# Kernel optimization log

Measured on AMD Instinct MI355X. Metric: run time of the kernel, lower is better.

## Reference

```python
import jax, jax.numpy as jnp
import numpy as np

N, K = 16384, 25
D_SELF, D_NEIGH, D_LINK, D_OUT = 256, 256, 64, 256


def _glorot(key, shape):
    fan = shape[0] if len(shape) == 1 else (shape[0] + shape[1])
    limit = np.sqrt(6.0 / fan).astype(np.float32)
    return jax.random.uniform(key, shape, jnp.float32, -limit, limit)


def setup_inputs() -> dict:
    key = jax.random.key(0)
    ks = jax.random.split(key, 10)
    return {
        "self_vecs": jax.random.normal(ks[0], (N, D_SELF), jnp.float32),
        "neigh_vecs": jax.random.normal(ks[1], (N, K, D_NEIGH), jnp.float32),
        "link_vecs": jax.random.normal(ks[2], (N, K, D_LINK), jnp.float32),
        # keep probs away from 0 to avoid huge 1/p values
        "select_probs": jax.random.uniform(ks[3], (N, K), jnp.float32) * 0.9 + 0.1,
        # Gate parameters (weight vectors)
        "g_self_w": _glorot(ks[4], (D_SELF,)),
        "g_neigh_w": _glorot(ks[5], (D_NEIGH,)),
        "g_link_w": _glorot(ks[6], (D_LINK,)),
        # Aggregator parameters
        "W_link": _glorot(ks[7], (D_LINK, D_NEIGH)),
        "W_self": _glorot(ks[8], (D_SELF, D_OUT)),
        "W_neigh": _glorot(ks[9], (D_NEIGH, D_OUT)),
    }


def reference(self_vecs, neigh_vecs, link_vecs, select_probs,
              g_self_w, g_neigh_w, g_link_w, W_link, W_self, W_neigh):
    # dropout = 0.0 -> identity
    # Gate: sigmoid(trans_self[:, None] + trans_neigh + trans_link)  -> [N, K]
    trans_self = self_vecs @ g_self_w                                  # [N]
    trans_neigh = jnp.einsum('nkd,d->nk', neigh_vecs, g_neigh_w)       # [N, K]
    trans_link = jnp.einsum('nkl,l->nk', link_vecs, g_link_w)          # [N, K]
    gate = jax.nn.sigmoid(trans_self[:, None] + trans_neigh + trans_link)

    # link-conditioned amplification of neighbor features
    trans_links = jax.nn.sigmoid(jnp.einsum('nkl,ld->nkd', link_vecs, W_link))  # [N, K, D_NEIGH]
    amplified = neigh_vecs * trans_links

    # select_probs provided -> gate/prob weighting and mean over neighbors
    w = gate / select_probs                                            # [N, K]
    expected = jnp.mean(amplified * w[..., None], axis=-2)             # [N, D_NEIGH]

    from_self = self_vecs @ W_self                                     # [N, D_OUT]
    from_neighs = expected @ W_neigh                                   # [N, D_OUT]
    out = jnp.concatenate([from_self, from_neighs], axis=-1)           # concat combination
    return jax.nn.relu(out)
```

## Files before the change

kernel.cpp:

```cpp
#include <hip/hip_runtime.h>

#define DEV __device__ __forceinline__

typedef __bf16 bf16;
typedef bf16 bf16x4 __attribute__((ext_vector_type(4)));
typedef bf16 bf16x8 __attribute__((ext_vector_type(8)));
typedef float f32x4 __attribute__((ext_vector_type(4)));

constexpr int N_NODES = 16384;
constexpr int KN = 25;
constexpr int DS = 256, DN = 256, DL = 64;

constexpr size_t WS_WLT  = 0;
constexpr size_t WS_WCAT = 32768;
constexpr size_t WS_EXP  = 32768 + 262144;

DEV float sigmoid_fast(float x) {
    return __builtin_amdgcn_rcpf(1.0f + __builtin_amdgcn_exp2f(-1.44269504088896341f * x));
}

__global__ void prep_kernel(const float* __restrict__ W_link,
                            const float* __restrict__ W_self,
                            const float* __restrict__ W_neigh,
                            bf16* __restrict__ wlT, bf16* __restrict__ wcat) {
    int tid = blockIdx.x * blockDim.x + threadIdx.x;
    int stride = gridDim.x * blockDim.x;
    for (int i = tid; i < DL * DN; i += stride) {
        int d = i >> 6, l = i & 63;
        wlT[i] = (bf16)W_link[l * DN + d];
    }
    for (int i = tid; i < 512 * 256; i += stride) {
        int j = i >> 8, kk = i & 255;
        float v = (j < 256) ? W_self[kk * 256 + j] : W_neigh[kk * 256 + (j - 256)];
        wcat[i] = (bf16)v;
    }
}

constexpr int NB = 8;
constexpr int LPAD = 72;

__global__ __launch_bounds__(256, 2)
void fused_agg_kernel(const float* __restrict__ self_vecs,
                      const float* __restrict__ neigh_vecs,
                      const float* __restrict__ link_vecs,
                      const float* __restrict__ probs,
                      const float* __restrict__ g_self_w,
                      const float* __restrict__ g_neigh_w,
                      const float* __restrict__ g_link_w,
                      const bf16* __restrict__ wlT,
                      bf16* __restrict__ exp_out) {
    __shared__ bf16 WT[256 * LPAD];
    __shared__ bf16 LK[32 * LPAD];
    __shared__ float wk_s[32];

    const int tid = threadIdx.x;
    const int lane = tid & 63;
    const int w = tid >> 6;
    const int c = lane & 15;
    const int q = lane >> 4;

    for (int it = 0; it < 16; ++it) {
        int idx = it * 1024 + tid * 4;
        int d = idx >> 6, l = idx & 63;
        *(bf16x4*)&WT[d * LPAD + l] = *(const bf16x4*)&wlT[idx];
    }

    f32x4 gsw = *(const f32x4*)&g_self_w[lane * 4];
    f32x4 glw = *(const f32x4*)&g_link_w[c * 4];
    float gn16[16];
#pragma unroll
    for (int u = 0; u < 4; ++u) {
        f32x4 t = *(const f32x4*)&g_neigh_w[c * 16 + u * 4];
        gn16[u * 4 + 0] = t[0]; gn16[u * 4 + 1] = t[1];
        gn16[u * 4 + 2] = t[2]; gn16[u * 4 + 3] = t[3];
    }

    for (int it = 0; it < NB; ++it) {
        const int n = blockIdx.x * NB + it;
        const float* nbase = neigh_vecs + (size_t)n * KN * DN;

        f32x4 sv = *(const f32x4*)&self_vecs[(size_t)n * DS + lane * 4];
        float ts = sv[0] * gsw[0] + sv[1] * gsw[1] + sv[2] * gsw[2] + sv[3] * gsw[3];
#pragma unroll
        for (int off = 1; off < 64; off <<= 1) ts += __shfl_xor(ts, off);

        float tl[2];
#pragma unroll
        for (int i = 0; i < 2; ++i) {
            int row = w * 8 + i * 4 + q;
            bool valid = row < KN;
            f32x4 lv = {0.f, 0.f, 0.f, 0.f};
            if (valid) lv = *(const f32x4*)&link_vecs[((size_t)n * KN + row) * DL + c * 4];
            bf16x4 lb; lb[0] = (bf16)lv[0]; lb[1] = (bf16)lv[1]; lb[2] = (bf16)lv[2]; lb[3] = (bf16)lv[3];
            *(bf16x4*)&LK[row * LPAD + c * 4] = lb;
            float p = lv[0] * glw[0] + lv[1] * glw[1] + lv[2] * glw[2] + lv[3] * glw[3];
            p += __shfl_xor(p, 1); p += __shfl_xor(p, 2);
            p += __shfl_xor(p, 4); p += __shfl_xor(p, 8);
            tl[i] = p;
        }

#pragma unroll
        for (int i = 0; i < 2; ++i) {
            int row = w * 8 + i * 4 + q;
            bool valid = row < KN;
            float tn = 0.f;
            if (valid) {
                const float* nr = nbase + row * DN + c * 16;
#pragma unroll
                for (int u = 0; u < 4; ++u) {
                    f32x4 nv = *(const f32x4*)&nr[u * 4];
                    tn += nv[0] * gn16[u * 4 + 0] + nv[1] * gn16[u * 4 + 1]
                        + nv[2] * gn16[u * 4 + 2] + nv[3] * gn16[u * 4 + 3];
                }
            }
            tn += __shfl_xor(tn, 1); tn += __shfl_xor(tn, 2);
            tn += __shfl_xor(tn, 4); tn += __shfl_xor(tn, 8);
            float wkv = 0.f;
            if (valid) {
                float pr = probs[n * KN + row];
                wkv = sigmoid_fast(ts + tn + tl[i]) * __builtin_amdgcn_rcpf(pr * 25.0f);
            }
            if (c == 0) wk_s[row] = wkv;
        }

        __syncthreads();

        float wkA[4], wkB[4];
#pragma unroll
        for (int r = 0; r < 4; ++r) { wkA[r] = wk_s[q * 4 + r]; wkB[r] = wk_s[q * 4 + r + 16]; }
        const int kc = q * 8;
        bf16x8 a00 = *(const bf16x8*)&LK[c * LPAD + kc];
        bf16x8 a01 = *(const bf16x8*)&LK[c * LPAD + kc + 32];
        bf16x8 a10 = *(const bf16x8*)&LK[(c + 16) * LPAD + kc];
        bf16x8 a11 = *(const bf16x8*)&LK[(c + 16) * LPAD + kc + 32];

#pragma unroll
        for (int t = 0; t < 4; ++t) {
            const int d0 = w * 64 + t * 16;
            bf16x8 b0 = *(const bf16x8*)&WT[(d0 + c) * LPAD + kc];
            bf16x8 b1 = *(const bf16x8*)&WT[(d0 + c) * LPAD + kc + 32];
            f32x4 acc0 = {0.f, 0.f, 0.f, 0.f};
            f32x4 acc1 = {0.f, 0.f, 0.f, 0.f};
            acc0 = __builtin_amdgcn_mfma_f32_16x16x32_bf16(a00, b0, acc0, 0, 0, 0);
            acc0 = __builtin_amdgcn_mfma_f32_16x16x32_bf16(a01, b1, acc0, 0, 0, 0);
            acc1 = __builtin_amdgcn_mfma_f32_16x16x32_bf16(a10, b0, acc1, 0, 0, 0);
            acc1 = __builtin_amdgcn_mfma_f32_16x16x32_bf16(a11, b1, acc1, 0, 0, 0);

            const int col = d0 + c;
            const float* np = nbase + col;
            float part = 0.f;
#pragma unroll
            for (int r = 0; r < 4; ++r) {
                int rowA = q * 4 + r;
                int rowB = rowA + 16; if (rowB > 24) rowB = 24;
                float sA = sigmoid_fast(acc0[r]);
                float sB = sigmoid_fast(acc1[r]);
                part += sA * wkA[r] * np[rowA * DN];
                part += sB * wkB[r] * np[rowB * DN];
            }
            part += __shfl_xor(part, 16);
            part += __shfl_xor(part, 32);
            if (q == 0) exp_out[(size_t)n * DN + col] = (bf16)part;
        }
        __syncthreads();
    }
}

constexpr int BPAD = 72;

__global__ __launch_bounds__(256, 2)
void out_gemm_kernel(const float* __restrict__ self_vecs,
                     const bf16* __restrict__ exp_in,
                     const bf16* __restrict__ wcat,
                     float* __restrict__ out) {
    __shared__ bf16 As[64 * BPAD];
    __shared__ bf16 Bs[64 * BPAD];
    const int tid = threadIdx.x;
    const int lane = tid & 63;
    const int w = tid >> 6;
    const int c = lane & 15, q = lane >> 4;
    const int wm = w >> 1, wn = w & 1;
    const int m0 = blockIdx.x * 64;
    const int j0 = blockIdx.y * 64;
    const bool use_exp = j0 >= 256;

    f32x4 acc[2][2];
#pragma unroll
    for (int i = 0; i < 2; ++i)
#pragma unroll
        for (int j = 0; j < 2; ++j) acc[i][j] = (f32x4){0.f, 0.f, 0.f, 0.f};

    const int srow = tid >> 4;
    const int scol = (tid & 15) * 4;

    for (int ks = 0; ks < 4; ++ks) {
        const int k0 = ks * 64;
        __syncthreads();
#pragma unroll
        for (int i = 0; i < 4; ++i) {
            int row = srow + i * 16;
            if (use_exp) {
                *(bf16x4*)&As[row * BPAD + scol] =
                    *(const bf16x4*)&exp_in[(size_t)(m0 + row) * 256 + k0 + scol];
            } else {
                f32x4 v = *(const f32x4*)&self_vecs[(size_t)(m0 + row) * 256 + k0 + scol];
                bf16x4 b; b[0] = (bf16)v[0]; b[1] = (bf16)v[1]; b[2] = (bf16)v[2]; b[3] = (bf16)v[3];
                *(bf16x4*)&As[row * BPAD + scol] = b;
            }
            *(bf16x4*)&Bs[row * BPAD + scol] =
                *(const bf16x4*)&wcat[(size_t)(j0 + row) * 256 + k0 + scol];
        }
        __syncthreads();
        const int kc = q * 8;
#pragma unroll
        for (int i = 0; i < 2; ++i) {
            bf16x8 a0 = *(const bf16x8*)&As[(wm * 32 + i * 16 + c) * BPAD + kc];
            bf16x8 a1 = *(const bf16x8*)&As[(wm * 32 + i * 16 + c) * BPAD + kc + 32];
#pragma unroll
            for (int j = 0; j < 2; ++j) {
                bf16x8 b0 = *(const bf16x8*)&Bs[(wn * 32 + j * 16 + c) * BPAD + kc];
                bf16x8 b1 = *(const bf16x8*)&Bs[(wn * 32 + j * 16 + c) * BPAD + kc + 32];
                acc[i][j] = __builtin_amdgcn_mfma_f32_16x16x32_bf16(a0, b0, acc[i][j], 0, 0, 0);
                acc[i][j] = __builtin_amdgcn_mfma_f32_16x16x32_bf16(a1, b1, acc[i][j], 0, 0, 0);
            }
        }
    }

#pragma unroll
    for (int i = 0; i < 2; ++i)
#pragma unroll
        for (int j = 0; j < 2; ++j)
#pragma unroll
            for (int r = 0; r < 4; ++r) {
                int row = m0 + wm * 32 + i * 16 + q * 4 + r;
                int col = j0 + wn * 32 + j * 16 + c;
                float v = acc[i][j][r];
                out[(size_t)row * 512 + col] = v > 0.f ? v : 0.f;
            }
}

extern "C" void kernel_launch(void* const* d_in, const int* in_sizes, int n_in,
                              void* d_out, int out_size, void* d_ws, size_t ws_size,
                              hipStream_t stream) {
    const float* self_vecs  = (const float*)d_in[0];
    const float* neigh_vecs = (const float*)d_in[1];
    const float* link_vecs  = (const float*)d_in[2];
    const float* probs      = (const float*)d_in[3];
    const float* g_self_w   = (const float*)d_in[4];
    const float* g_neigh_w  = (const float*)d_in[5];
    const float* g_link_w   = (const float*)d_in[6];
    const float* W_link     = (const float*)d_in[7];
    const float* W_self     = (const float*)d_in[8];
    const float* W_neigh    = (const float*)d_in[9];
    float* out = (float*)d_out;

    char* ws = (char*)d_ws;
    bf16* wlT  = (bf16*)(ws + WS_WLT);
    bf16* wcat = (bf16*)(ws + WS_WCAT);
    bf16* expb = (bf16*)(ws + WS_EXP);

    prep_kernel<<<dim3(128), dim3(256), 0, stream>>>(W_link, W_self, W_neigh, wlT, wcat);
    fused_agg_kernel<<<dim3(N_NODES / NB), dim3(256), 0, stream>>>(
        self_vecs, neigh_vecs, link_vecs, probs, g_self_w, g_neigh_w, g_link_w, wlT, expb);
    out_gemm_kernel<<<dim3(256, 8), dim3(256), 0, stream>>>(self_vecs, expb, wcat, out);
}
```

Before: 721.0 us.

## Assign one wavefront per node and remove per-node block barriers

Reorganizes the aggregation kernel so each wavefront processes whole nodes independently, computing the full link-transform GEMM itself and staging sigmoid results in a per-wave LDS buffer. Neighbor rows are then streamed with coalesced float4 loads, fusing the gate dot product, amplification and weighted sum in one pass. This removes block-wide __syncthreads per node and the strided per-column neighbor reads. In exchange it adds a full-wave shuffle reduction per neighbor and serializes the neighbor loop within a wave.

```diff
diff --git a/kernel.cpp b/kernel.cpp
--- a/kernel.cpp
+++ b/kernel.cpp
@@ -17,6 +17,10 @@
 
 DEV float sigmoid_fast(float x) {
     return __builtin_amdgcn_rcpf(1.0f + __builtin_amdgcn_exp2f(-1.44269504088896341f * x));
+}
+
+DEV float dot4(f32x4 a, f32x4 b) {
+    return a[0] * b[0] + a[1] * b[1] + a[2] * b[2] + a[3] * b[3];
 }
 
 __global__ void prep_kernel(const float* __restrict__ W_link,
@@ -36,8 +40,9 @@
     }
 }
 
-constexpr int NB = 8;
-constexpr int LPAD = 72;
+constexpr int NPW = 8;
+constexpr int WTS = 72;
+constexpr int STS = 264;
 
 __global__ __launch_bounds__(256, 2)
 void fused_agg_kernel(const float* __restrict__ self_vecs,
@@ -49,9 +54,8 @@
                       const float* __restrict__ g_link_w,
                       const bf16* __restrict__ wlT,
                       bf16* __restrict__ exp_out) {
-    __shared__ bf16 WT[256 * LPAD];
-    __shared__ bf16 LK[32 * LPAD];
-    __shared__ float wk_s[32];
+    __shared__ bf16 WT[256 * WTS];
+    __shared__ bf16 ST[4][16 * STS];
 
     const int tid = threadIdx.x;
     const int lane = tid & 63;
@@ -59,110 +63,97 @@
     const int c = lane & 15;
     const int q = lane >> 4;
 
-    for (int it = 0; it < 16; ++it) {
-        int idx = it * 1024 + tid * 4;
+    for (int i = 0; i < 16; ++i) {
+        int idx = i * 1024 + tid * 4;
         int d = idx >> 6, l = idx & 63;
-        *(bf16x4*)&WT[d * LPAD + l] = *(const bf16x4*)&wlT[idx];
-    }
+        *(bf16x4*)&WT[d * WTS + l] = *(const bf16x4*)&wlT[idx];
+    }
+    __syncthreads();
 
     f32x4 gsw = *(const f32x4*)&g_self_w[lane * 4];
-    f32x4 glw = *(const f32x4*)&g_link_w[c * 4];
-    float gn16[16];
-#pragma unroll
-    for (int u = 0; u < 4; ++u) {
-        f32x4 t = *(const f32x4*)&g_neigh_w[c * 16 + u * 4];
-        gn16[u * 4 + 0] = t[0]; gn16[u * 4 + 1] = t[1];
-        gn16[u * 4 + 2] = t[2]; gn16[u * 4 + 3] = t[3];
-    }
-
-    for (int it = 0; it < NB; ++it) {
-        const int n = blockIdx.x * NB + it;
+    f32x4 gnw = *(const f32x4*)&g_neigh_w[lane * 4];
+    f32x4 glw0a = *(const f32x4*)&g_link_w[q * 8];
+    f32x4 glw0b = *(const f32x4*)&g_link_w[q * 8 + 4];
+    f32x4 glw1a = *(const f32x4*)&g_link_w[32 + q * 8];
+    f32x4 glw1b = *(const f32x4*)&g_link_w[32 + q * 8 + 4];
+
+    for (int it = 0; it < NPW; ++it) {
+        const int n = (blockIdx.x * 4 + w) * NPW + it;
         const float* nbase = neigh_vecs + (size_t)n * KN * DN;
+        const float* lbase = link_vecs + (size_t)n * KN * DL;
 
         f32x4 sv = *(const f32x4*)&self_vecs[(size_t)n * DS + lane * 4];
-        float ts = sv[0] * gsw[0] + sv[1] * gsw[1] + sv[2] * gsw[2] + sv[3] * gsw[3];
+        float ts = dot4(sv, gsw);
 #pragma unroll
         for (int off = 1; off < 64; off <<= 1) ts += __shfl_xor(ts, off);
 
-        float tl[2];
-#pragma unroll
-        for (int i = 0; i < 2; ++i) {
-            int row = w * 8 + i * 4 + q;
-            bool valid = row < KN;
-            f32x4 lv = {0.f, 0.f, 0.f, 0.f};
-            if (valid) lv = *(const f32x4*)&link_vecs[((size_t)n * KN + row) * DL + c * 4];
-            bf16x4 lb; lb[0] = (bf16)lv[0]; lb[1] = (bf16)lv[1]; lb[2] = (bf16)lv[2]; lb[3] = (bf16)lv[3];
-            *(bf16x4*)&LK[row * LPAD + c * 4] = lb;
-            float p = lv[0] * glw[0] + lv[1] * glw[1] + lv[2] * glw[2] + lv[3] * glw[3];
-            p += __shfl_xor(p, 1); p += __shfl_xor(p, 2);
-            p += __shfl_xor(p, 4); p += __shfl_xor(p, 8);
-            tl[i] = p;
-        }
-
-#pragma unroll
-        for (int i = 0; i < 2; ++i) {
-            int row = w * 8 + i * 4 + q;
-            bool valid = row < KN;
-            float tn = 0.f;
-            if (valid) {
-                const float* nr = nbase + row * DN + c * 16;
-#pragma unroll
-                for (int u = 0; u < 4; ++u) {
-                    f32x4 nv = *(const f32x4*)&nr[u * 4];
-                    tn += nv[0] * gn16[u * 4 + 0] + nv[1] * gn16[u * 4 + 1]
-                        + nv[2] * gn16[u * 4 + 2] + nv[3] * gn16[u * 4 + 3];
-                }
-            }
-            tn += __shfl_xor(tn, 1); tn += __shfl_xor(tn, 2);
-            tn += __shfl_xor(tn, 4); tn += __shfl_xor(tn, 8);
-            float wkv = 0.f;
-            if (valid) {
-                float pr = probs[n * KN + row];
-                wkv = sigmoid_fast(ts + tn + tl[i]) * __builtin_amdgcn_rcpf(pr * 25.0f);
-            }
-            if (c == 0) wk_s[row] = wkv;
-        }
-
-        __syncthreads();
-
-        float wkA[4], wkB[4];
-#pragma unroll
-        for (int r = 0; r < 4; ++r) { wkA[r] = wk_s[q * 4 + r]; wkB[r] = wk_s[q * 4 + r + 16]; }
-        const int kc = q * 8;
-        bf16x8 a00 = *(const bf16x8*)&LK[c * LPAD + kc];
-        bf16x8 a01 = *(const bf16x8*)&LK[c * LPAD + kc + 32];
-        bf16x8 a10 = *(const bf16x8*)&LK[(c + 16) * LPAD + kc];
-        bf16x8 a11 = *(const bf16x8*)&LK[(c + 16) * LPAD + kc + 32];
-
-#pragma unroll
-        for (int t = 0; t < 4; ++t) {
-            const int d0 = w * 64 + t * 16;
-            bf16x8 b0 = *(const bf16x8*)&WT[(d0 + c) * LPAD + kc];
-            bf16x8 b1 = *(const bf16x8*)&WT[(d0 + c) * LPAD + kc + 32];
-            f32x4 acc0 = {0.f, 0.f, 0.f, 0.f};
-            f32x4 acc1 = {0.f, 0.f, 0.f, 0.f};
-            acc0 = __builtin_amdgcn_mfma_f32_16x16x32_bf16(a00, b0, acc0, 0, 0, 0);
-            acc0 = __builtin_amdgcn_mfma_f32_16x16x32_bf16(a01, b1, acc0, 0, 0, 0);
-            acc1 = __builtin_amdgcn_mfma_f32_16x16x32_bf16(a10, b0, acc1, 0, 0, 0);
-            acc1 = __builtin_amdgcn_mfma_f32_16x16x32_bf16(a11, b1, acc1, 0, 0, 0);
-
-            const int col = d0 + c;
-            const float* np = nbase + col;
-            float part = 0.f;
-#pragma unroll
-            for (int r = 0; r < 4; ++r) {
-                int rowA = q * 4 + r;
-                int rowB = rowA + 16; if (rowB > 24) rowB = 24;
-                float sA = sigmoid_fast(acc0[r]);
-                float sB = sigmoid_fast(acc1[r]);
-                part += sA * wkA[r] * np[rowA * DN];
-                part += sB * wkB[r] * np[rowB * DN];
-            }
-            part += __shfl_xor(part, 16);
-            part += __shfl_xor(part, 32);
-            if (q == 0) exp_out[(size_t)n * DN + col] = (bf16)part;
-        }
-        __syncthreads();
+        f32x4 v0 = *(const f32x4*)&lbase[c * DL + q * 8];
+        f32x4 v1 = *(const f32x4*)&lbase[c * DL + q * 8 + 4];
+        f32x4 v2 = *(const f32x4*)&lbase[c * DL + 32 + q * 8];
+        f32x4 v3 = *(const f32x4*)&lbase[c * DL + 32 + q * 8 + 4];
+        const int rB = c + 16;
+        const f32x4 z = {0.f, 0.f, 0.f, 0.f};
+        f32x4 u0 = z, u1 = z, u2 = z, u3 = z;
+        if (rB < KN) {
+            u0 = *(const f32x4*)&lbase[rB * DL + q * 8];
+            u1 = *(const f32x4*)&lbase[rB * DL + q * 8 + 4];
+            u2 = *(const f32x4*)&lbase[rB * DL + 32 + q * 8];
+            u3 = *(const f32x4*)&lbase[rB * DL + 32 + q * 8 + 4];
+        }
+        bf16x8 a00, a01, a10, a11;
+#pragma unroll
+        for (int j = 0; j < 4; ++j) {
+            a00[j] = (bf16)v0[j]; a00[j + 4] = (bf16)v1[j];
+            a01[j] = (bf16)v2[j]; a01[j + 4] = (bf16)v3[j];
+            a10[j] = (bf16)u0[j]; a10[j + 4] = (bf16)u1[j];
+            a11[j] = (bf16)u2[j]; a11[j + 4] = (bf16)u3[j];
+        }
+        float tlA = dot4(v0, glw0a) + dot4(v1, glw0b) + dot4(v2, glw1a) + dot4(v3, glw1b);
+        tlA += __shfl_xor(tlA, 16); tlA += __shfl_xor(tlA, 32);
+        float tlB = dot4(u0, glw0a) + dot4(u1, glw0b) + dot4(u2, glw1a) + dot4(u3, glw1b);
+        tlB += __shfl_xor(tlB, 16); tlB += __shfl_xor(tlB, 32);
+
+        float gk = ts + ((lane & 63) < 16 ? tlA : tlB);
+        float pv = (lane < KN) ? probs[n * KN + lane] : 1.0f;
+        float wden = __builtin_amdgcn_rcpf(pv * 25.0f);
+
+        f32x4 accd = z;
+
+#pragma unroll
+        for (int half = 0; half < 2; ++half) {
+            const bf16x8 aF0 = half ? a10 : a00;
+            const bf16x8 aF1 = half ? a11 : a01;
+#pragma unroll
+            for (int t = 0; t < 16; ++t) {
+                bf16x8 b0 = *(const bf16x8*)&WT[(t * 16 + c) * WTS + q * 8];
+                bf16x8 b1 = *(const bf16x8*)&WT[(t * 16 + c) * WTS + 32 + q * 8];
+                f32x4 acc = z;
+                acc = __builtin_amdgcn_mfma_f32_16x16x32_bf16(aF0, b0, acc, 0, 0, 0);
+                acc = __builtin_amdgcn_mfma_f32_16x16x32_bf16(aF1, b1, acc, 0, 0, 0);
+#pragma unroll
+                for (int r = 0; r < 4; ++r)
+                    ST[w][(q * 4 + r) * STS + t * 16 + c] = (bf16)sigmoid_fast(acc[r]);
+            }
+            const int k0 = half * 16;
+            const int k1 = half ? KN : 16;
+#pragma unroll
+            for (int k = k0; k < k1; ++k) {
+                f32x4 nv = *(const f32x4*)&nbase[(size_t)k * DN + lane * 4];
+                bf16x4 s4 = *(const bf16x4*)&ST[w][(k - k0) * STS + lane * 4];
+                float tn = dot4(nv, gnw);
+#pragma unroll
+                for (int off = 1; off < 64; off <<= 1) tn += __shfl_xor(tn, off);
+                float wkk = sigmoid_fast(tn + __shfl(gk, k)) * __shfl(wden, k);
+#pragma unroll
+                for (int j = 0; j < 4; ++j)
+                    accd[j] += nv[j] * (float)s4[j] * wkk;
+            }
+        }
+
+        bf16x4 eo;
+#pragma unroll
+        for (int j = 0; j < 4; ++j) eo[j] = (bf16)accd[j];
+        *(bf16x4*)&exp_out[(size_t)n * DN + lane * 4] = eo;
     }
 }
 
@@ -260,7 +251,7 @@
     bf16* expb = (bf16*)(ws + WS_EXP);
 
     prep_kernel<<<dim3(128), dim3(256), 0, stream>>>(W_link, W_self, W_neigh, wlT, wcat);
-    fused_agg_kernel<<<dim3(N_NODES / NB), dim3(256), 0, stream>>>(
+    fused_agg_kernel<<<dim3(N_NODES / (4 * NPW)), dim3(256), 0, stream>>>(
         self_vecs, neigh_vecs, link_vecs, probs, g_self_w, g_neigh_w, g_link_w, wlT, expb);
     out_gemm_kernel<<<dim3(256, 8), dim3(256), 0, stream>>>(self_vecs, expb, wcat, out);
 }
```

Measured after the change: 669.7 us. 1.08x faster.
